# Kernel optimization log

Measured on AMD Instinct MI355X. Metric: run time of the kernel, lower is better.

The kernel has to match this reference:

```python
import jax, jax.numpy as jnp
import numpy as np

# ---- config (from init_kwargs) ----
PRE_NMS_THRESH = 0.05
PRE_NMS_TOP_N = 1000
NMS_THRESH = 0.6
FPN_POST_NMS_TOP_N = 100
MIN_SIZE = 0.0
FPN_STRIDES = (8.0, 16.0, 32.0, 64.0, 128.0)
TO_REMOVE = 1.0

M = 2097152   # total FPN points over the batch
N = 16        # images
C = 11        # classes incl. background column (zeroed)


def setup_inputs() -> dict:
    key = jax.random.key(0)
    k1, k2, k3, k4, k5, k6 = jax.random.split(key, 6)
    locations = jax.random.uniform(k1, (M, 2), jnp.float32) * 1024.0
    box_cls = jax.random.normal(k2, (M, C), jnp.float32) * 2.0
    box_regression = jax.random.uniform(k3, (M, 4), jnp.float32) * 4.0
    centerness = jax.random.normal(k4, (M, 1), jnp.float32)
    levels = jax.random.randint(k5, (M,), 0, len(FPN_STRIDES), jnp.int32)
    batch_indices = jnp.sort(jax.random.randint(k6, (M,), 0, N, jnp.int32))
    image_sizes = jnp.tile(jnp.array([[800, 1333]], jnp.int32), (N, 1))  # (h, w)
    return dict(locations=locations, levels=levels, batch_indices=batch_indices,
                box_cls=box_cls, box_regression=box_regression,
                centerness=centerness, image_sizes=image_sizes)


def _iou_matrix(b):
    x1, y1, x2, y2 = b[:, 0], b[:, 1], b[:, 2], b[:, 3]
    area = jnp.clip(x2 - x1 + TO_REMOVE, 0.0) * jnp.clip(y2 - y1 + TO_REMOVE, 0.0)
    xx1 = jnp.maximum(x1[:, None], x1[None, :])
    yy1 = jnp.maximum(y1[:, None], y1[None, :])
    xx2 = jnp.minimum(x2[:, None], x2[None, :])
    yy2 = jnp.minimum(y2[:, None], y2[None, :])
    inter = jnp.clip(xx2 - xx1 + TO_REMOVE, 0.0) * jnp.clip(yy2 - yy1 + TO_REMOVE, 0.0)
    return inter / jnp.maximum(area[:, None] + area[None, :] - inter, 1e-9)


def _greedy_nms(iou, keep0):
    # boxes assumed sorted by descending score; keep0 = validity mask
    K = keep0.shape[0]
    idx = jnp.arange(K)
    def step(keep, i):
        sup = (iou[i] > NMS_THRESH) & (idx > i) & keep[i]
        return keep & ~sup, None
    keep, _ = jax.lax.scan(step, keep0, jnp.arange(K))
    return keep


def _fcos_post(locations, box_cls, box_regression, centerness,
               levels, batch_indices, image_sizes):
    strides = jnp.asarray(FPN_STRIDES, box_regression.dtype)
    reg = box_regression * strides[levels][:, None]          # norm_reg_targets=True
    scores = jax.nn.sigmoid(box_cls) * jax.nn.sigmoid(centerness)  # [M,C]
    scores = scores.at[:, -1].set(0.0)                       # kill background column
    boxes_all = jnp.concatenate([locations - reg[:, :2],
                                 locations + reg[:, 2:]], axis=-1)  # [M,4]

    def per_image(args):
        i, hw = args
        m = (batch_indices == i)[:, None] & (scores > PRE_NMS_THRESH)
        flat = jnp.where(m, scores, 0.0).reshape(-1)          # [M*C]
        topv, topi = jax.lax.top_k(flat, PRE_NMS_TOP_N)       # sorted desc
        pt = topi // C
        cl = (topi % C + 1).astype(jnp.int32)                 # labels = class + 1
        b = boxes_all[pt]                                     # [K,4]
        v0 = topv > 0.0                                       # pad entries -> invalid
        sc = jnp.sqrt(jnp.where(v0, topv, 1.0)) * v0          # sqrt(score), safe at pads
        h = hw[0].astype(b.dtype); w = hw[1].astype(b.dtype)
        x1 = jnp.clip(b[:, 0], 0.0, w - TO_REMOVE)            # clip_to_image
        y1 = jnp.clip(b[:, 1], 0.0, h - TO_REMOVE)
        x2 = jnp.clip(b[:, 2], 0.0, w - TO_REMOVE)
        y2 = jnp.clip(b[:, 3], 0.0, h - TO_REMOVE)
        b = jnp.stack([x1, y1, x2, y2], axis=-1)
        ws = x2 - x1 + TO_REMOVE; hs = y2 - y1 + TO_REMOVE    # remove_small_boxes
        keep0 = v0 & (ws >= MIN_SIZE) & (hs >= MIN_SIZE)
        # class-aware NMS via coordinate offset trick
        max_coord = jnp.max(jnp.where(keep0[:, None], b, 0.0))
        boff = jax.lax.stop_gradient(b + (cl.astype(b.dtype) * (max_coord + 1.0))[:, None])
        keep = _greedy_nms(_iou_matrix(boff), keep0)
        sck = jnp.where(keep, sc, 0.0)
        fv, fi = jax.lax.top_k(sck, FPN_POST_NMS_TOP_N)       # fpn_post_nms_top_n
        return b[fi], fv, cl[fi], fv > 0.0

    boxes_o, scores_o, labels_o, valid_o = jax.lax.map(
        per_image, (jnp.arange(N), image_sizes))
    return boxes_o, scores_o, labels_o, valid_o


def reference(locations, levels, batch_indices, box_cls, box_regression,
              centerness, image_sizes):
    return _fcos_post(locations, box_cls, box_regression, centerness,
                      levels, batch_indices, image_sizes)
```

## Files before the change

kernel.cpp:

```cpp
#include <hip/hip_runtime.h>
#include <math.h>

#pragma clang fp contract(off)

#define MPTS   2097152
#define NIMG   16
#define NCLS   11
#define CUTB   0x3F000000u
#define NB2    1026
#define NB2P   1040
#define MARG   96u
#define CAP    4096
#define TOPN   1000
#define OUTN   100
#define LCAP   64

typedef unsigned long long u64;

#define SUPW_PER_IMG 8704
__device__ __forceinline__ int chunk_base(int c) {
    return 64 * (16 * c - (c * (c - 1)) / 2);
}

__device__ inline float sigx(float x) {
    float e = (float)exp(-(double)x);
    return 1.0f / (1.0f + e);
}
__device__ inline float sigf(float x) {
    float e = __expf(-x);
    return __builtin_amdgcn_rcpf(1.0f + e);
}
__device__ inline float bfr(float x) {
    unsigned u = __float_as_uint(x);
    unsigned r = (u + 0x7FFFu + ((u >> 16) & 1u)) & 0xFFFF0000u;
    return __uint_as_float(r);
}
__device__ __forceinline__ u64 rdlane64(u64 v, int l) {
    unsigned lo = (unsigned)__builtin_amdgcn_readlane((int)(unsigned)(v & 0xFFFFFFFFull), l);
    unsigned hi = (unsigned)__builtin_amdgcn_readlane((int)(unsigned)(v >> 32), l);
    return ((u64)hi << 32) | (u64)lo;
}

__global__ __launch_bounds__(1024)
void k_hist(const float4* __restrict__ cls4, const float* __restrict__ ctr,
            const int* __restrict__ batch, unsigned* __restrict__ ghist) {
    __shared__ unsigned hist[NB2];
    __shared__ int simg;
    const int F4  = MPTS * NCLS / 4;
    const int FPB = F4 / 512;
    int f0 = blockIdx.x * FPB;
    int t = threadIdx.x;
    for (int i = t; i < NB2; i += 1024) hist[i] = 0;
    if (t == 0) simg = batch[(unsigned)(4u * (unsigned)f0) / NCLS];
    __syncthreads();
    int bi = simg;
    unsigned pc = 0xFFFFFFFFu;
    float sfc = 0.0f;
    int bc = 0;
    for (int f = f0 + t; f < f0 + FPB; f += 1024) {
        float4 v = cls4[f];
        float va[4] = {v.x, v.y, v.z, v.w};
        unsigned e0 = 4u * (unsigned)f;
        #pragma unroll
        for (int j = 0; j < 4; j++) {
            float ck = va[j];
            if (ck <= 0.0f) continue;
            unsigned e = e0 + (unsigned)j;
            unsigned p = e / NCLS;
            unsigned k = e - p * NCLS;
            if (k == 10u) continue;
            if (p != pc) {
                pc = p; sfc = sigf(ctr[p]); bc = batch[p];
            }
            unsigned fb = __float_as_uint(sigf(ck) * sfc);
            if (fb < CUTB) continue;
            unsigned bin = (fb - CUTB) >> 13;
            if (bin >= NB2) bin = NB2 - 1;
            if (bc == bi) atomicAdd(&hist[bin], 1u);
            else          atomicAdd(&ghist[(size_t)bc * NB2P + bin], 1u);
        }
    }
    __syncthreads();
    unsigned* gh = ghist + (size_t)bi * NB2P;
    for (int i = t; i < NB2; i += 1024) {
        unsigned v2 = hist[i];
        if (v2) atomicAdd(&gh[i], v2);
    }
}

__global__ void k_thresh(const unsigned* __restrict__ ghist, unsigned* __restrict__ thrbuf) {
    int img = blockIdx.x;
    const unsigned* h = ghist + (size_t)img * NB2P;
    __shared__ unsigned psum[256];
    int t = threadIdx.x;
    unsigned s = 0;
    int base = t * 5;
    for (int i = 0; i < 5; i++) { int b = base + i; if (b < NB2) s += h[b]; }
    psum[t] = s;
    __syncthreads();
    if (t == 0) {
        unsigned run = 0; int B = 0;
        for (int u = 205; u >= 0; u--) {
            if (run + psum[u] >= (unsigned)TOPN) {
                int btop = u * 5 + 4; if (btop > NB2 - 1) btop = NB2 - 1;
                for (int b = btop; b >= u * 5; b--) {
                    run += h[b];
                    if (run >= (unsigned)TOPN) { B = b; break; }
                }
                break;
            }
            run += psum[u];
        }
        unsigned TB = CUTB + ((unsigned)B << 13) - MARG;
        thrbuf[2 * img] = TB;
        thrbuf[2 * img + 1] = __float_as_uint(__uint_as_float(TB) * 0.998f);
    }
}

__global__ __launch_bounds__(256)
void k_collect(const float4* __restrict__ cls4, const float* __restrict__ ctr,
               const int* __restrict__ batch, const unsigned* __restrict__ thrbuf,
               unsigned* __restrict__ gcnt, unsigned long long* __restrict__ cand) {
    __shared__ unsigned sTB[NIMG];
    __shared__ float sSCR[NIMG];
    __shared__ u64 lbuf[NIMG][LCAP];
    __shared__ unsigned lcnt[NIMG];
    __shared__ unsigned lbase[NIMG];
    int t = threadIdx.x;
    if (t < NIMG) {
        sTB[t]  = thrbuf[2 * t];
        sSCR[t] = __uint_as_float(thrbuf[2 * t + 1]);
        lcnt[t] = 0;
    }
    __syncthreads();
    const int F4  = MPTS * NCLS / 4;
    const int FPB = F4 / 2048;
    int f0 = blockIdx.x * FPB;
    unsigned pc = 0xFFFFFFFFu;
    float cgs = 0.0f, sfc = 0.0f, sxc = 0.0f, scrc = 0.0f;
    bool havex = false;
    int bc = 0; unsigned TBc = 0;
    for (int f = f0 + t; f < f0 + FPB; f += 256) {
        float4 v = cls4[f];
        float va[4] = {v.x, v.y, v.z, v.w};
        unsigned e0 = 4u * (unsigned)f;
        #pragma unroll
        for (int j = 0; j < 4; j++) {
            float ck = va[j];
            if (ck <= -0.001f) continue;
            unsigned e = e0 + (unsigned)j;
            unsigned p = e / NCLS;
            unsigned k = e - p * NCLS;
            if (k == 10u) continue;
            if (p != pc) {
                pc = p; cgs = ctr[p]; bc = batch[p];
                sfc = sigf(cgs); havex = false;
                TBc = sTB[bc]; scrc = sSCR[bc];
            }
            float sf = sigf(ck) * sfc;
            if (sf > scrc) {
                if (!havex) { sxc = sigx(cgs); havex = true; }
                float s = sigx(ck) * sxc;
                unsigned bits = __float_as_uint(s);
                if (bits >= TBc && s > 0.05f) {
                    u64 key = ((u64)bits << 32) | (u64)(0xFFFFFFFFu - e);
                    unsigned slot = atomicAdd(&lcnt[bc], 1u);
                    if (slot < LCAP) lbuf[bc][slot] = key;
                    else {
                        unsigned pos = atomicAdd(&gcnt[bc * 16], 1u);
                        if (pos < CAP) cand[(size_t)bc * CAP + pos] = key;
                    }
                }
            }
        }
    }
    __syncthreads();
    if (t < NIMG) {
        unsigned n = lcnt[t]; if (n > LCAP) n = LCAP;
        lcnt[t] = n;
        lbase[t] = n ? atomicAdd(&gcnt[t * 16], n) : 0u;
    }
    __syncthreads();
    for (int s = t; s < NIMG * LCAP; s += 256) {
        int im = s >> 6;
        int sl = s & (LCAP - 1);
        if (sl < (int)lcnt[im]) {
            unsigned pos = lbase[im] + (unsigned)sl;
            if (pos < CAP) cand[(size_t)im * CAP + pos] = lbuf[im][sl];
        }
    }
}

__global__ __launch_bounds__(1024)
void k_rank(const u64* __restrict__ cand, const unsigned* __restrict__ gcnt,
            u64* __restrict__ srt) {
    int img = blockIdx.x >> 2;
    int sub = blockIdx.x & 3;
    __shared__ u64 keys[CAP];
    unsigned n = gcnt[img * 16]; if (n > CAP) n = CAP;
    for (int i = threadIdx.x; i < (int)n; i += 1024)
        keys[i] = cand[(size_t)img * CAP + i];
    __syncthreads();
    int i = sub * 1024 + (int)threadIdx.x;
    if (i < (int)n) {
        u64 me = keys[i];
        int rank = 0;
        int j = 0;
        for (; j + 4 <= (int)n; j += 4) {
            rank += (keys[j]     > me);
            rank += (keys[j + 1] > me);
            rank += (keys[j + 2] > me);
            rank += (keys[j + 3] > me);
        }
        for (; j < (int)n; j++) rank += (keys[j] > me);
        if (rank < TOPN) srt[(size_t)img * TOPN + rank] = me;
    }
}

__global__ __launch_bounds__(256)
void k_build(const u64* __restrict__ srt,
             const float* __restrict__ loc, const float* __restrict__ breg,
             const int* __restrict__ levels, const int* __restrict__ imsz,
             float* __restrict__ bx, float* __restrict__ sc, int* __restrict__ cl,
             unsigned* __restrict__ k0, float* __restrict__ bo, float* __restrict__ ar) {
    int img = blockIdx.x;
    __shared__ float red[256];
    __shared__ float smc;
    float wmax = (float)imsz[img * 2 + 1] - 1.0f;
    float hmax = (float)imsz[img * 2 + 0] - 1.0f;
    float lmax = 0.0f;
    for (int r = threadIdx.x; r < TOPN; r += 256) {
        u64 kv = srt[(size_t)img * TOPN + r];
        unsigned bits = (unsigned)(kv >> 32);
        unsigned idx = 0xFFFFFFFFu - (unsigned)(kv & 0xFFFFFFFFull);
        float v = __uint_as_float(bits);
        bool v0 = (kv != 0ull) && (v > 0.0f);
        if (!v0) idx = 0;
        unsigned pt = idx / NCLS;
        int c = (int)(idx - pt * NCLS);
        float lx = loc[(size_t)pt * 2 + 0], ly = loc[(size_t)pt * 2 + 1];
        float st = (float)(8 << levels[pt]);
        float r0 = breg[(size_t)pt * 4 + 0] * st;
        float r1 = breg[(size_t)pt * 4 + 1] * st;
        float r2 = breg[(size_t)pt * 4 + 2] * st;
        float r3 = breg[(size_t)pt * 4 + 3] * st;
        float x1 = lx - r0, y1 = ly - r1, x2 = lx + r2, y2 = ly + r3;
        x1 = fminf(fmaxf(x1, 0.0f), wmax);
        y1 = fminf(fmaxf(y1, 0.0f), hmax);
        x2 = fminf(fmaxf(x2, 0.0f), wmax);
        y2 = fminf(fmaxf(y2, 0.0f), hmax);
        float wss = (x2 - x1) + 1.0f, hss = (y2 - y1) + 1.0f;
        bool keep = v0 && (wss >= 0.0f) && (hss >= 0.0f);
        size_t ob = (size_t)img * TOPN + r;
        bx[ob * 4 + 0] = x1; bx[ob * 4 + 1] = y1;
        bx[ob * 4 + 2] = x2; bx[ob * 4 + 3] = y2;
        sc[ob] = v0 ? sqrtf(v) : 0.0f;
        cl[ob] = c + 1;
        k0[ob] = keep ? 1u : 0u;
        if (keep) lmax = fmaxf(lmax, fmaxf(fmaxf(x1, y1), fmaxf(x2, y2)));
    }
    red[threadIdx.x] = lmax; __syncthreads();
    for (int sft = 128; sft > 0; sft >>= 1) {
        if ((int)threadIdx.x < sft) red[threadIdx.x] = fmaxf(red[threadIdx.x], red[threadIdx.x + sft]);
        __syncthreads();
    }
    if (threadIdx.x == 0) smc = red[0];
    __syncthreads();
    float off1 = smc + 1.0f;
    for (int r = threadIdx.x; r < TOPN; r += 256) {
        size_t ob = (size_t)img * TOPN + r;
        float o = (float)cl[ob] * off1;
        float x1 = bx[ob * 4 + 0] + o, y1 = bx[ob * 4 + 1] + o;
        float x2 = bx[ob * 4 + 2] + o, y2 = bx[ob * 4 + 3] + o;
        bo[ob * 4 + 0] = x1; bo[ob * 4 + 1] = y1;
        bo[ob * 4 + 2] = x2; bo[ob * 4 + 3] = y2;
        float aw = fmaxf((x2 - x1) + 1.0f, 0.0f);
        float ah = fmaxf((y2 - y1) + 1.0f, 0.0f);
        ar[ob] = aw * ah;
    }
}

__global__ __launch_bounds__(1024)
void k_iou(const float* __restrict__ bo, const float* __restrict__ ar,
           u64* __restrict__ sup) {
    int img = blockIdx.x >> 4;
    int c   = blockIdx.x & 15;
    __shared__ float sx1[1024], sy1[1024], sx2[1024], sy2[1024], sa[1024];
    int tid = threadIdx.x;
    {
        int i = tid;
        if (i < TOPN) {
            size_t ob = (size_t)img * TOPN + i;
            sx1[i] = bo[ob * 4 + 0]; sy1[i] = bo[ob * 4 + 1];
            sx2[i] = bo[ob * 4 + 2]; sy2[i] = bo[ob * 4 + 3];
            sa[i]  = ar[ob];
        } else {
            sx1[i] = 0.0f; sy1[i] = 0.0f; sx2[i] = 0.0f; sy2[i] = 0.0f; sa[i] = 0.0f;
        }
    }
    __syncthreads();
    int width = 16 - c;
    int items = 64 * width;
    u64* supc = sup + (size_t)img * SUPW_PER_IMG + chunk_base(c);
    for (int it = tid; it < items; it += 1024) {
        int r  = it & 63;
        int wq = c + (it >> 6);
        int i  = c * 64 + r;
        if (i >= TOPN) continue;
        float x1 = sx1[i], y1 = sy1[i], x2 = sx2[i], y2 = sy2[i], a = sa[i];
        int j0 = wq * 64;
        u64 m = 0ull;
        #pragma unroll 8
        for (int jj = 0; jj < 64; jj++) {
            int j = j0 + jj;
            float xx1 = fmaxf(x1, sx1[j]);
            float yy1 = fmaxf(y1, sy1[j]);
            float xx2 = fminf(x2, sx2[j]);
            float yy2 = fminf(y2, sy2[j]);
            float iw = fmaxf((xx2 - xx1) + 1.0f, 0.0f);
            float ih = fmaxf((yy2 - yy1) + 1.0f, 0.0f);
            float inter = iw * ih;
            float den = fmaxf((a + sa[j]) - inter, 1e-9f);
            if (inter / den > 0.6f) m |= (1ull << jj);
        }
        u64 vm = ~0ull;
        if (wq == c) vm = (r >= 63) ? 0ull : (~0ull << (r + 1));
        int rem = TOPN - j0;
        if (rem < 64) vm &= (rem <= 0) ? 0ull : ((1ull << rem) - 1ull);
        supc[(size_t)r * width + (wq - c)] = m & vm;
    }
}

__device__ __forceinline__ void scan_pref(const u64* __restrict__ supi, int rg, int w, int t,
                                          int C, u64 (&V)[16], u64 &anyV, u64 &dmy) {
    int wd = 16 - C;
    const u64* rb = supi + chunk_base(C) + (rg << 4) * wd - C + w;
    u64 a = 0ull;
    #pragma unroll
    for (int i = 0; i < 16; i++) {
        u64 x = rb[i * wd];
        V[i] = (w >= C) ? x : 0ull;
        a |= V[i];
    }
    anyV = a;
    dmy = supi[chunk_base(C) + (size_t)t * wd];
}

__device__ __forceinline__ void scan_step(int rg, int w, int C,
                                          u64 (&V)[16], u64 anyV, u64 dmy,
                                          u64 &kw_local) {
    u64 m = rdlane64(kw_local, C);
    u64 act = __ballot(dmy != 0ull) & m;
    while (act) {
        int r = __builtin_ctzll(act);
        u64 d = rdlane64(dmy, r);
        m &= ~d;
        act &= act - 1ull;
        act &= m;
    }
    if (__ballot(anyV != 0ull)) {
        u64 loc = 0ull;
        #pragma unroll
        for (int i = 0; i < 16; i++) {
            int row = (rg << 4) + i;
            loc |= V[i] & ((u64)0 - ((m >> row) & 1ull));
        }
        u64 t1 = loc | __shfl_xor(loc, 16);
        u64 t2 = t1 | __shfl_xor(t1, 32);
        kw_local = ((w == C) ? m : kw_local) & ~t2;
    } else if (w == C) {
        kw_local = m;
    }
}

__global__ __launch_bounds__(64)
void k_scan_out(const u64* __restrict__ sup, const unsigned* __restrict__ k0,
                const float* __restrict__ bx, const float* __restrict__ sc,
                const int* __restrict__ cl, float* __restrict__ out) {
    int img = blockIdx.x;
    int t = threadIdx.x;
    int rg = t >> 4, w = t & 15;
    const u64* supi = sup + (size_t)img * SUPW_PER_IMG;

    u64 kw_local = 0ull;
    #pragma unroll
    for (int q = 0; q < 16; q++) {
        int i = (q << 6) + t;
        unsigned vv = (i < TOPN) ? k0[(size_t)img * TOPN + i] : 0u;
        u64 bal = __ballot(vv != 0u);
        if (w == q) kw_local = bal;
    }

    u64 vA[16], vB[16], anyA, anyB, dA, dB;
    scan_pref(supi, rg, w, t, 0, vA, anyA, dA);
    for (int c = 0; c < 16; c += 2) {
        scan_pref(supi, rg, w, t, c + 1, vB, anyB, dB);
        scan_step(rg, w, c, vA, anyA, dA, kw_local);
        if (c + 2 < 16) scan_pref(supi, rg, w, t, c + 2, vA, anyA, dA);
        scan_step(rg, w, c + 1, vB, anyB, dB, kw_local);
    }

    u64 kws[16];
    #pragma unroll
    for (int q = 0; q < 16; q++) kws[q] = rdlane64(kw_local, q);

    __shared__ int fi[OUTN];
    int total_k = 0;
    #pragma unroll
    for (int q = 0; q < 16; q++) total_k += __popcll(kws[q]);
    int snk = total_k < OUTN ? total_k : OUTN;
    int run = 0;
    #pragma unroll
    for (int q = 0; q < 16; q++) {
        u64 word = kws[q];
        int i = (q << 6) + t;
        int kb = __popcll(word & ((1ull << t) - 1ull));
        bool kept = ((word >> t) & 1ull) != 0ull;
        int krank = run + kb;
        if (kept) {
            if (krank < OUTN) fi[krank] = i;
        } else if (i < TOPN) {
            int slot = snk + (i - krank);
            if (slot < OUTN) fi[slot] = i;
        }
        run += __popcll(word);
    }
    __syncthreads();

    for (int q = t; q < OUTN; q += 64) {
        int r = fi[q];
        bool kv = q < snk;
        size_t ob = (size_t)img * TOPN + r;
        float sv = kv ? sc[ob] : 0.0f;
        int o = img * OUTN + q;
        out[o * 4 + 0] = bfr(bx[ob * 4 + 0]);
        out[o * 4 + 1] = bfr(bx[ob * 4 + 1]);
        out[o * 4 + 2] = bfr(bx[ob * 4 + 2]);
        out[o * 4 + 3] = bfr(bx[ob * 4 + 3]);
        out[6400 + o] = bfr(sv);
        out[8000 + o] = (float)cl[ob];
        out[9600 + o] = (sv > 0.0f) ? 1.0f : 0.0f;
    }
}

extern "C" void kernel_launch(void* const* d_in, const int* in_sizes, int n_in,
                              void* d_out, int out_size, void* d_ws, size_t ws_size,
                              hipStream_t stream) {
    const float* loc    = (const float*)d_in[0];
    const int*   levels = (const int*)d_in[1];
    const int*   batch  = (const int*)d_in[2];
    const float* cls    = (const float*)d_in[3];
    const float* breg   = (const float*)d_in[4];
    const float* ctr    = (const float*)d_in[5];
    const int*   imsz   = (const int*)d_in[6];

    char* ws = (char*)d_ws;
    unsigned long long* cand   = (unsigned long long*)(ws + 0);
    unsigned*           ghist  = (unsigned*)(ws + 524288);
    u64*                srt    = (u64*)(ws + 591872);
    float*              bx     = (float*)(ws + 852096);
    float*              bo     = (float*)(ws + 1108096);
    float*              ar     = (float*)(ws + 1364096);
    float*              sc     = (float*)(ws + 1428096);
    int*                cl     = (int*)(ws + 1492096);
    unsigned*           k0     = (unsigned*)(ws + 1556096);
    unsigned*           gcnt   = (unsigned*)(ws + 1620096);
    unsigned*           thrbuf = (unsigned*)(ws + 1621120);
    u64*                sup    = (u64*)(ws + 1703936);
    float* out = (float*)d_out;

    hipMemsetAsync(ghist, 0, 16 * NB2P * 4, stream);
    hipMemsetAsync(gcnt, 0, 1024, stream);
    hipMemsetAsync(srt, 0, 16 * TOPN * 8, stream);
    k_hist    <<<512,  1024, 0, stream>>>((const float4*)cls, ctr, batch, ghist);
    k_thresh  <<<16,   256,  0, stream>>>(ghist, thrbuf);
    k_collect <<<2048, 256,  0, stream>>>((const float4*)cls, ctr, batch, thrbuf, gcnt, cand);
    k_rank    <<<64,   1024, 0, stream>>>(cand, gcnt, srt);
    k_build   <<<16,   256,  0, stream>>>(srt, loc, breg, levels, imsz,
                                          bx, sc, cl, k0, bo, ar);
    k_iou     <<<256,  1024, 0, stream>>>(bo, ar, sup);
    k_scan_out<<<16,   64,   0, stream>>>(sup, k0, bx, sc, cl, out);
}
```

Baseline: 320.3 us.

## Record high-score candidates during histogram pass and fuse rank with box build

During the histogram pass, elements whose score clears a fixed pre-threshold have their indices recorded per image. The collect kernel then reads only these records instead of rescanning the full class tensor, and falls back to the full scan if the threshold is too low or the buffer overflows. Rank and box build are merged into one kernel per image that keeps the sorted keys in shared memory, which removes a memset and a global round trip. The cost is extra atomics in the histogram pass, and the fused rank now runs on 16 blocks instead of 64, which reduces its parallelism.

```diff
diff --git a/kernel.cpp b/kernel.cpp
--- a/kernel.cpp
+++ b/kernel.cpp
@@ -7,6 +7,9 @@
 #define NIMG   16
 #define NCLS   11
 #define CUTB   0x3F000000u
+#define PREB   0x3F4CCC00u
+#define BSAFE  620
+#define PRECAP 14336
 #define NB2    1026
 #define NB2P   1040
 #define MARG   96u
@@ -43,15 +46,18 @@
 
 __global__ __launch_bounds__(1024)
 void k_hist(const float4* __restrict__ cls4, const float* __restrict__ ctr,
-            const int* __restrict__ batch, unsigned* __restrict__ ghist) {
+            const int* __restrict__ batch, unsigned* __restrict__ ghist,
+            unsigned* __restrict__ gcnt, unsigned* __restrict__ prerec) {
     __shared__ unsigned hist[NB2];
+    __shared__ unsigned pA[512], pB[256];
+    __shared__ unsigned cA, cB, bA;
     __shared__ int simg;
     const int F4  = MPTS * NCLS / 4;
     const int FPB = F4 / 512;
     int f0 = blockIdx.x * FPB;
     int t = threadIdx.x;
     for (int i = t; i < NB2; i += 1024) hist[i] = 0;
-    if (t == 0) simg = batch[(unsigned)(4u * (unsigned)f0) / NCLS];
+    if (t == 0) { simg = batch[(unsigned)(4u * (unsigned)f0) / NCLS]; cA = 0; cB = 0; }
     __syncthreads();
     int bi = simg;
     unsigned pc = 0xFFFFFFFFu;
@@ -78,6 +84,23 @@
             if (bin >= NB2) bin = NB2 - 1;
             if (bc == bi) atomicAdd(&hist[bin], 1u);
             else          atomicAdd(&ghist[(size_t)bc * NB2P + bin], 1u);
+            if (fb >= PREB) {
+                if (bc == bi) {
+                    unsigned sl = atomicAdd(&cA, 1u);
+                    if (sl < 512u) pA[sl] = e;
+                    else {
+                        unsigned pos = atomicAdd(&gcnt[bi * 16 + 8], 1u);
+                        if (pos < PRECAP) prerec[(size_t)bi * PRECAP + pos] = e;
+                    }
+                } else {
+                    unsigned sl = atomicAdd(&cB, 1u);
+                    if (sl < 256u) pB[sl] = e;
+                    else {
+                        unsigned pos = atomicAdd(&gcnt[bc * 16 + 8], 1u);
+                        if (pos < PRECAP) prerec[(size_t)bc * PRECAP + pos] = e;
+                    }
+                }
+            }
         }
     }
     __syncthreads();
@@ -86,9 +109,27 @@
         unsigned v2 = hist[i];
         if (v2) atomicAdd(&gh[i], v2);
     }
-}
-
-__global__ void k_thresh(const unsigned* __restrict__ ghist, unsigned* __restrict__ thrbuf) {
+    if (t == 0) {
+        unsigned nn = cA; if (nn > 512u) nn = 512u;
+        cA = nn;
+        bA = nn ? atomicAdd(&gcnt[bi * 16 + 8], nn) : 0u;
+    }
+    __syncthreads();
+    for (unsigned i = t; i < cA; i += 1024) {
+        unsigned pos = bA + i;
+        if (pos < PRECAP) prerec[(size_t)bi * PRECAP + pos] = pA[i];
+    }
+    unsigned nb = cB; if (nb > 256u) nb = 256u;
+    for (unsigned i = t; i < nb; i += 1024) {
+        unsigned e2 = pB[i];
+        int img2 = batch[e2 / NCLS];
+        unsigned pos = atomicAdd(&gcnt[img2 * 16 + 8], 1u);
+        if (pos < PRECAP) prerec[(size_t)img2 * PRECAP + pos] = e2;
+    }
+}
+
+__global__ void k_thresh(const unsigned* __restrict__ ghist, unsigned* __restrict__ thrbuf,
+                         unsigned* __restrict__ gcnt) {
     int img = blockIdx.x;
     const unsigned* h = ghist + (size_t)img * NB2P;
     __shared__ unsigned psum[256];
@@ -114,19 +155,66 @@
         unsigned TB = CUTB + ((unsigned)B << 13) - MARG;
         thrbuf[2 * img] = TB;
         thrbuf[2 * img + 1] = __float_as_uint(__uint_as_float(TB) * 0.998f);
+        if (B < BSAFE || gcnt[img * 16 + 8] > PRECAP) atomicOr(&gcnt[1], 1u);
     }
 }
 
 __global__ __launch_bounds__(256)
-void k_collect(const float4* __restrict__ cls4, const float* __restrict__ ctr,
-               const int* __restrict__ batch, const unsigned* __restrict__ thrbuf,
-               unsigned* __restrict__ gcnt, unsigned long long* __restrict__ cand) {
+void k_collect(const float4* __restrict__ cls4, const float* __restrict__ clsf,
+               const float* __restrict__ ctr, const int* __restrict__ batch,
+               const unsigned* __restrict__ thrbuf, unsigned* __restrict__ gcnt,
+               const unsigned* __restrict__ prerec, unsigned long long* __restrict__ cand) {
+    int t = threadIdx.x;
+    if (gcnt[1] == 0u) {
+        if (blockIdx.x >= 256) return;
+        int img = blockIdx.x >> 4;
+        int sub = blockIdx.x & 15;
+        unsigned TB = thrbuf[2 * img];
+        float scr = __uint_as_float(thrbuf[2 * img + 1]);
+        unsigned n = gcnt[img * 16 + 8];
+        __shared__ u64 l2[512];
+        __shared__ unsigned c2, b2;
+        if (t == 0) c2 = 0;
+        __syncthreads();
+        const unsigned* pr = prerec + (size_t)img * PRECAP;
+        for (unsigned i = (unsigned)(sub * 256 + t); i < n; i += 4096) {
+            unsigned e = pr[i];
+            unsigned p = e / NCLS;
+            float ck = clsf[e];
+            float cgs = ctr[p];
+            float sf = sigf(ck) * sigf(cgs);
+            if (sf > scr) {
+                float s = sigx(ck) * sigx(cgs);
+                unsigned bits = __float_as_uint(s);
+                if (bits >= TB && s > 0.05f) {
+                    u64 key = ((u64)bits << 32) | (u64)(0xFFFFFFFFu - e);
+                    unsigned sl = atomicAdd(&c2, 1u);
+                    if (sl < 512u) l2[sl] = key;
+                    else {
+                        unsigned pos = atomicAdd(&gcnt[img * 16], 1u);
+                        if (pos < CAP) cand[(size_t)img * CAP + pos] = key;
+                    }
+                }
+            }
+        }
+        __syncthreads();
+        if (t == 0) {
+            unsigned nn = c2; if (nn > 512u) nn = 512u;
+            c2 = nn;
+            b2 = nn ? atomicAdd(&gcnt[img * 16], nn) : 0u;
+        }
+        __syncthreads();
+        for (unsigned sl = t; sl < c2; sl += 256) {
+            unsigned pos = b2 + sl;
+            if (pos < CAP) cand[(size_t)img * CAP + pos] = l2[sl];
+        }
+        return;
+    }
     __shared__ unsigned sTB[NIMG];
     __shared__ float sSCR[NIMG];
     __shared__ u64 lbuf[NIMG][LCAP];
     __shared__ unsigned lcnt[NIMG];
     __shared__ unsigned lbase[NIMG];
-    int t = threadIdx.x;
     if (t < NIMG) {
         sTB[t]  = thrbuf[2 * t];
         sSCR[t] = __uint_as_float(thrbuf[2 * t + 1]);
@@ -192,18 +280,23 @@
 }
 
 __global__ __launch_bounds__(1024)
-void k_rank(const u64* __restrict__ cand, const unsigned* __restrict__ gcnt,
-            u64* __restrict__ srt) {
-    int img = blockIdx.x >> 2;
-    int sub = blockIdx.x & 3;
+void k_rankb(const u64* __restrict__ cand, const unsigned* __restrict__ gcnt,
+             const float* __restrict__ loc, const float* __restrict__ breg,
+             const int* __restrict__ levels, const int* __restrict__ imsz,
+             float* __restrict__ bx, float* __restrict__ sc, int* __restrict__ cl,
+             unsigned* __restrict__ k0, float* __restrict__ bo, float* __restrict__ ar) {
+    int img = blockIdx.x;
+    int t = threadIdx.x;
     __shared__ u64 keys[CAP];
+    __shared__ u64 srtl[TOPN];
+    __shared__ float red[1024];
+    __shared__ float smc;
     unsigned n = gcnt[img * 16]; if (n > CAP) n = CAP;
-    for (int i = threadIdx.x; i < (int)n; i += 1024)
-        keys[i] = cand[(size_t)img * CAP + i];
-    __syncthreads();
-    int i = sub * 1024 + (int)threadIdx.x;
-    if (i < (int)n) {
-        u64 me = keys[i];
+    for (int i = t; i < (int)n; i += 1024) keys[i] = cand[(size_t)img * CAP + i];
+    for (int i = t; i < TOPN; i += 1024) srtl[i] = 0ull;
+    __syncthreads();
+    for (int ii = t; ii < (int)n; ii += 1024) {
+        u64 me = keys[ii];
         int rank = 0;
         int j = 0;
         for (; j + 4 <= (int)n; j += 4) {
@@ -213,24 +306,14 @@
             rank += (keys[j + 3] > me);
         }
         for (; j < (int)n; j++) rank += (keys[j] > me);
-        if (rank < TOPN) srt[(size_t)img * TOPN + rank] = me;
-    }
-}
-
-__global__ __launch_bounds__(256)
-void k_build(const u64* __restrict__ srt,
-             const float* __restrict__ loc, const float* __restrict__ breg,
-             const int* __restrict__ levels, const int* __restrict__ imsz,
-             float* __restrict__ bx, float* __restrict__ sc, int* __restrict__ cl,
-             unsigned* __restrict__ k0, float* __restrict__ bo, float* __restrict__ ar) {
-    int img = blockIdx.x;
-    __shared__ float red[256];
-    __shared__ float smc;
+        if (rank < TOPN) srtl[rank] = me;
+    }
+    __syncthreads();
     float wmax = (float)imsz[img * 2 + 1] - 1.0f;
     float hmax = (float)imsz[img * 2 + 0] - 1.0f;
     float lmax = 0.0f;
-    for (int r = threadIdx.x; r < TOPN; r += 256) {
-        u64 kv = srt[(size_t)img * TOPN + r];
+    for (int r = t; r < TOPN; r += 1024) {
+        u64 kv = srtl[r];
         unsigned bits = (unsigned)(kv >> 32);
         unsigned idx = 0xFFFFFFFFu - (unsigned)(kv & 0xFFFFFFFFull);
         float v = __uint_as_float(bits);
@@ -259,15 +342,15 @@
         k0[ob] = keep ? 1u : 0u;
         if (keep) lmax = fmaxf(lmax, fmaxf(fmaxf(x1, y1), fmaxf(x2, y2)));
     }
-    red[threadIdx.x] = lmax; __syncthreads();
-    for (int sft = 128; sft > 0; sft >>= 1) {
-        if ((int)threadIdx.x < sft) red[threadIdx.x] = fmaxf(red[threadIdx.x], red[threadIdx.x + sft]);
+    red[t] = lmax; __syncthreads();
+    for (int sft = 512; sft > 0; sft >>= 1) {
+        if (t < sft) red[t] = fmaxf(red[t], red[t + sft]);
         __syncthreads();
     }
-    if (threadIdx.x == 0) smc = red[0];
+    if (t == 0) smc = red[0];
     __syncthreads();
     float off1 = smc + 1.0f;
-    for (int r = threadIdx.x; r < TOPN; r += 256) {
+    for (int r = t; r < TOPN; r += 1024) {
         size_t ob = (size_t)img * TOPN + r;
         float o = (float)cl[ob] * off1;
         float x1 = bx[ob * 4 + 0] + o, y1 = bx[ob * 4 + 1] + o;
@@ -457,7 +540,6 @@
     char* ws = (char*)d_ws;
     unsigned long long* cand   = (unsigned long long*)(ws + 0);
     unsigned*           ghist  = (unsigned*)(ws + 524288);
-    u64*                srt    = (u64*)(ws + 591872);
     float*              bx     = (float*)(ws + 852096);
     float*              bo     = (float*)(ws + 1108096);
     float*              ar     = (float*)(ws + 1364096);
@@ -467,16 +549,15 @@
     unsigned*           gcnt   = (unsigned*)(ws + 1620096);
     unsigned*           thrbuf = (unsigned*)(ws + 1621120);
     u64*                sup    = (u64*)(ws + 1703936);
+    unsigned*           prerec = (unsigned*)(ws + 1703936);
     float* out = (float*)d_out;
 
     hipMemsetAsync(ghist, 0, 16 * NB2P * 4, stream);
     hipMemsetAsync(gcnt, 0, 1024, stream);
-    hipMemsetAsync(srt, 0, 16 * TOPN * 8, stream);
-    k_hist    <<<512,  1024, 0, stream>>>((const float4*)cls, ctr, batch, ghist);
-    k_thresh  <<<16,   256,  0, stream>>>(ghist, thrbuf);
-    k_collect <<<2048, 256,  0, stream>>>((const float4*)cls, ctr, batch, thrbuf, gcnt, cand);
-    k_rank    <<<64,   1024, 0, stream>>>(cand, gcnt, srt);
-    k_build   <<<16,   256,  0, stream>>>(srt, loc, breg, levels, imsz,
+    k_hist    <<<512,  1024, 0, stream>>>((const float4*)cls, ctr, batch, ghist, gcnt, prerec);
+    k_thresh  <<<16,   256,  0, stream>>>(ghist, thrbuf, gcnt);
+    k_collect <<<2048, 256,  0, stream>>>((const float4*)cls, cls, ctr, batch, thrbuf, gcnt, prerec, cand);
+    k_rankb   <<<16,   1024, 0, stream>>>(cand, gcnt, loc, breg, levels, imsz,
                                           bx, sc, cl, k0, bo, ar);
     k_iou     <<<256,  1024, 0, stream>>>(bo, ar, sup);
     k_scan_out<<<16,   64,   0, stream>>>(sup, k0, bx, sc, cl, out);
```

Result: faster. 303.3 us (-5.3%).
